# Kernel tuning notes

Hardware: AMD Instinct MI355X
Metric: run time of the kernel (lower is better)

The kernel has to match this reference:

```python
import jax, jax.numpy as jnp
import numpy as np

N = 768  # length of time vector

def setup_inputs() -> dict:
    key = jax.random.key(0)
    ks = jax.random.split(key, 4)
    # time vector (sorted grid-like values, as in a GP time axis)
    x = jnp.sort(jax.random.uniform(ks[0], (N,), dtype=jnp.float32) * (6 * np.pi))
    # MLP params: Linear(2,1024) -> Sigmoid -> Linear(1024,128) -> ReLU -> Linear(128,1)
    W1 = jax.random.normal(ks[1], (1024, 2), dtype=jnp.float32) * (1.0 / np.sqrt(2.0))
    b1 = jnp.zeros((1024,), dtype=jnp.float32)
    W2 = jax.random.normal(ks[2], (128, 1024), dtype=jnp.float32) * (1.0 / np.sqrt(1024.0))
    b2 = jnp.zeros((128,), dtype=jnp.float32)
    W3 = jax.random.normal(ks[3], (1, 128), dtype=jnp.float32) * (1.0 / np.sqrt(128.0))
    b3 = jnp.zeros((1,), dtype=jnp.float32)
    return {"x": x, "W1": W1, "b1": b1, "W2": W2, "b2": b2, "W3": W3, "b3": b3}


def reference(x, W1, b1, W2, b2, W3, b3):
    n = x.shape[0]
    # all (i, j) with j >= i  -> n(n+1)/2 pairs; replaces the Python double loop
    iu, ju = jnp.triu_indices(n)
    pairs = jnp.stack([x[iu], x[ju]], axis=-1)            # [P, 2]
    h = jax.nn.sigmoid(pairs @ W1.T + b1)                 # [P, 1024]
    h = jax.nn.relu(h @ W2.T + b2)                        # [P, 128]
    v = (h @ W3.T + b3)[:, 0]                             # [P]
    # K starts as eye; upper triangle INCLUDING diagonal is overwritten
    K = jnp.eye(n, dtype=x.dtype).at[iu, ju].set(v)       # [n, n] upper-triangular
    return K.T @ K                                        # symmetric PSD covariance
```

## Files before the change

kernel.cpp:

```cpp
#include <hip/hip_runtime.h>
#include <hip/hip_bf16.h>

#define NN 768
#define MD 1024
#define NPAIR 295296
#define NPBLK 1154

typedef __attribute__((ext_vector_type(8))) short s16x8;
typedef __attribute__((ext_vector_type(4))) float f32x4;
typedef __attribute__((ext_vector_type(2))) __bf16 b16x2;

__device__ __forceinline__ ushort bf16_rn(float f) {
    uint u = __builtin_bit_cast(uint, f);
    u += 0x7FFFu + ((u >> 16) & 1u);
    return (ushort)(u >> 16);
}

__device__ __forceinline__ void ptoij(int p, int& io, int& jo) {
    const float disc = (float)(1537 * 1537 - 8 * p);
    int i = (int)((1537.0f - sqrtf(disc)) * 0.5f);
    i = i < 0 ? 0 : (i > 767 ? 767 : i);
    while (i > 0 && p < i * (1537 - i) / 2) --i;
    while (i < 767 && p >= (i + 1) * (1536 - i) / 2) ++i;
    io = i;
    jo = i + (p - i * (1537 - i) / 2);
}

#define GLOAD16(gsrc, ldst)                                                        \
    __builtin_amdgcn_global_load_lds(                                              \
        (const __attribute__((address_space(1))) void*)(gsrc),                     \
        (__attribute__((address_space(3))) void*)(ldst), 16, 0, 0)

__global__ __launch_bounds__(256) void w2bf16(const float* __restrict__ W2,
                                              ushort* __restrict__ WhiS)
{
    const int id = blockIdx.x * 256 + threadIdx.x;
    const int k = id >> 7;
    const int m = (id & 127) * 8;
    const float4 a = *reinterpret_cast<const float4*>(W2 + k * MD + m);
    const float4 b = *reinterpret_cast<const float4*>(W2 + k * MD + m + 4);
    const float w[8] = {a.x, a.y, a.z, a.w, b.x, b.y, b.z, b.w};
    s16x8 h;
#pragma unroll
    for (int e = 0; e < 8; ++e) h[e] = (short)bf16_rn(w[e]);
    const int c = m >> 6;
    const int mloc8 = (m >> 3) & 7;
    const int byte = (mloc8 * 16) ^ ((k & 7) << 4);
    const int off = c * 8192 + ((k * 128 + byte) >> 1);
    *reinterpret_cast<s16x8*>(&WhiS[off]) = h;
}

#define STAGE(cc, buf)                                                       \
    {                                                                        \
        const ushort* sh_ = WhiS + (cc) * 8192;                              \
        _Pragma("unroll")                                                    \
        for (int q_ = 0; q_ < 4; ++q_) {                                     \
            const int off_ = (wv * 4 + q_) * 512;                            \
            GLOAD16(sh_ + off_ + lane * 8, &Wh[buf][off_]);                  \
        }                                                                    \
    }

#define SIG_CHUNK(cc, dst)                                                   \
    {                                                                        \
        _Pragma("unroll")                                                    \
        for (int ks_ = 0; ks_ < 2; ++ks_) {                                  \
            const int m0_ = (cc) * 64 + ks_ * 32 + l4 * 8;                   \
            const f32x4 a0_ = *reinterpret_cast<const f32x4*>(&sa[m0_]);     \
            const f32x4 a1_ = *reinterpret_cast<const f32x4*>(&sa[m0_ + 4]); \
            const f32x4 c0_ = *reinterpret_cast<const f32x4*>(&sc[m0_]);     \
            const f32x4 c1_ = *reinterpret_cast<const f32x4*>(&sc[m0_ + 4]); \
            const f32x4 b0_ = *reinterpret_cast<const f32x4*>(&sb[m0_]);     \
            const f32x4 b1_ = *reinterpret_cast<const f32x4*>(&sb[m0_ + 4]); \
            _Pragma("unroll")                                                \
            for (int tm_ = 0; tm_ < 4; ++tm_) {                              \
                float s_[8];                                                 \
                _Pragma("unroll")                                            \
                for (int e_ = 0; e_ < 4; ++e_) {                             \
                    const float u0_ = fmaf(xia[tm_], a0_[e_], fmaf(xja[tm_], c0_[e_], b0_[e_])); \
                    const float u1_ = fmaf(xia[tm_], a1_[e_], fmaf(xja[tm_], c1_[e_], b1_[e_])); \
                    s_[e_]     = __builtin_amdgcn_rcpf(1.0f + __builtin_amdgcn_exp2f(u0_)); \
                    s_[e_ + 4] = __builtin_amdgcn_rcpf(1.0f + __builtin_amdgcn_exp2f(u1_)); \
                }                                                            \
                union { s16x8 v; uint u[4]; } fr_;                           \
                _Pragma("unroll")                                            \
                for (int h_ = 0; h_ < 4; ++h_) {                             \
                    b16x2 p_;                                                \
                    p_.x = (__bf16)s_[2 * h_];                               \
                    p_.y = (__bf16)s_[2 * h_ + 1];                           \
                    fr_.u[h_] = __builtin_bit_cast(uint, p_);                \
                }                                                            \
                dst[ks_][tm_] = fr_.v;                                       \
            }                                                                \
        }                                                                    \
    }

#define MFMA_STEP(buf, src)                                                  \
    {                                                                        \
        _Pragma("unroll")                                                    \
        for (int ks_ = 0; ks_ < 2; ++ks_) {                                  \
            _Pragma("unroll")                                                \
            for (int th_ = 0; th_ < 2; ++th_) {                              \
                s16x8 bh_[4];                                                \
                _Pragma("unroll")                                            \
                for (int tn_ = 0; tn_ < 4; ++tn_) {                          \
                    const int k_ = th_ * 64 + tn_ * 16 + l15;                \
                    const int byte_ = (ks_ * 64 + l4 * 16) ^ ((k_ & 7) << 4);\
                    const int idx_ = (k_ * 128 + byte_) >> 1;                \
                    bh_[tn_] = *reinterpret_cast<const s16x8*>(&Wh[buf][idx_]); \
                }                                                            \
                __builtin_amdgcn_s_setprio(1);                               \
                _Pragma("unroll")                                            \
                for (int tm_ = 0; tm_ < 4; ++tm_)                            \
                    _Pragma("unroll")                                        \
                    for (int tn_ = 0; tn_ < 4; ++tn_)                        \
                        acc[tm_][th_][tn_] = __builtin_amdgcn_mfma_f32_16x16x32_bf16( \
                            src[ks_][tm_], bh_[tn_], acc[tm_][th_][tn_], 0, 0, 0);    \
                __builtin_amdgcn_s_setprio(0);                               \
            }                                                                \
        }                                                                    \
    }

__global__ __launch_bounds__(256, 2) void mlp_pairs(
    const float* __restrict__ x,
    const float* __restrict__ W1, const float* __restrict__ b1,
    const ushort* __restrict__ WhiS,
    const float* __restrict__ b2, const float* __restrict__ W3,
    const float* __restrict__ b3, float* __restrict__ K)
{
    __shared__ __align__(16) float sa[MD], sc[MD], sb[MD];
    __shared__ __align__(16) ushort Wh[2][8192];

    const int t = threadIdx.x;
    const int lane = t & 63, wv = t >> 6;
    const int l15 = lane & 15, l4 = lane >> 4;

    const float NL2E = -1.4426950408889634f;
    for (int m = t; m < MD; m += 256) {
        const float2 w = reinterpret_cast<const float2*>(W1)[m];
        sa[m] = w.x * NL2E;
        sc[m] = w.y * NL2E;
        sb[m] = b1[m] * NL2E;
    }

    const int pairbase = blockIdx.x * 256 + wv * 64;

    float xia[4], xja[4];
#pragma unroll
    for (int tm = 0; tm < 4; ++tm) {
        const int p = pairbase + tm * 16 + l15;
        if (p < NPAIR) {
            int i, j;
            ptoij(p, i, j);
            xia[tm] = x[i];
            xja[tm] = x[j];
        } else {
            xia[tm] = 0.f;
            xja[tm] = 0.f;
        }
    }

    f32x4 acc[4][2][4];
#pragma unroll
    for (int a = 0; a < 4; ++a)
#pragma unroll
        for (int th = 0; th < 2; ++th)
#pragma unroll
            for (int b = 0; b < 4; ++b) acc[a][th][b] = (f32x4){0.f, 0.f, 0.f, 0.f};

    STAGE(0, 0);
    __syncthreads();

    s16x8 ah[2][4];
    for (int c = 0; c < 16; ++c) {
        if (c < 15) STAGE(c + 1, (c + 1) & 1);
        SIG_CHUNK(c, ah);
        MFMA_STEP(c & 1, ah);
        __syncthreads();
    }

    float w3v[2][4], b2v[2][4];
#pragma unroll
    for (int th = 0; th < 2; ++th)
#pragma unroll
        for (int tn = 0; tn < 4; ++tn) {
            const int k = th * 64 + tn * 16 + l15;
            w3v[th][tn] = W3[k];
            b2v[th][tn] = b2[k];
        }
    const float b3v = b3[0];
#pragma unroll
    for (int tm = 0; tm < 4; ++tm)
#pragma unroll
        for (int r = 0; r < 4; ++r) {
            float v = 0.f;
#pragma unroll
            for (int th = 0; th < 2; ++th)
#pragma unroll
                for (int tn = 0; tn < 4; ++tn)
                    v = fmaf(w3v[th][tn], fmaxf(acc[tm][th][tn][r] + b2v[th][tn], 0.f), v);
            v += __shfl_xor(v, 1, 16);
            v += __shfl_xor(v, 2, 16);
            v += __shfl_xor(v, 4, 16);
            v += __shfl_xor(v, 8, 16);
            if (l15 == 0) {
                const int p = pairbase + tm * 16 + l4 * 4 + r;
                if (p < NPAIR) {
                    int i, j;
                    ptoij(p, i, j);
                    K[i * NN + j] = v + b3v;
                }
            }
        }
}

#define MC 32
#define JT 128
#define SPAD 132
__global__ __launch_bounds__(256) void mlp_fill(
    const float* __restrict__ x,
    const float* __restrict__ W1, const float* __restrict__ b1,
    const float* __restrict__ W2, const float* __restrict__ b2,
    const float* __restrict__ W3, const float* __restrict__ b3,
    float* __restrict__ K)
{
    const int i  = blockIdx.y;
    const int j0 = blockIdx.x * JT;
    if (j0 + JT - 1 < i) return;
    __shared__ float sA[MD];
    __shared__ float sCw[MD];
    __shared__ float sxj[JT];
    __shared__ float S[MC][SPAD];
    __shared__ float W2t[MC][SPAD];
    const int t = threadIdx.x;
    const float xi = x[i];
    for (int m = t; m < MD; m += 256) {
        const float2 w = reinterpret_cast<const float2*>(W1)[m];
        sA[m]  = fmaf(xi, w.x, b1[m]);
        sCw[m] = w.y;
    }
    if (t < JT) sxj[t] = x[j0 + t];
    const int tk = t & 15;
    const int tj = t >> 4;
    float w3r[8], b2r[8];
#pragma unroll
    for (int kk = 0; kk < 8; kk++) {
        w3r[kk] = W3[tk * 8 + kk];
        b2r[kk] = b2[tk * 8 + kk];
    }
    float acc[8][8];
#pragma unroll
    for (int jj = 0; jj < 8; jj++)
#pragma unroll
        for (int kk = 0; kk < 8; kk++) acc[jj][kk] = 0.f;
    const int jx   = t & 127;
    const int mseg = (t >> 7) * 16;
    __syncthreads();
    const float xjv = sxj[jx];
    for (int m0 = 0; m0 < MD; m0 += MC) {
#pragma unroll
        for (int q = 0; q < 4; q++) {
            const int f   = t + q * 256;
            const int k   = f >> 3;
            const int mm4 = (f & 7) * 4;
            const float4 w = *reinterpret_cast<const float4*>(W2 + k * MD + m0 + mm4);
            W2t[mm4 + 0][k] = w.x;
            W2t[mm4 + 1][k] = w.y;
            W2t[mm4 + 2][k] = w.z;
            W2t[mm4 + 3][k] = w.w;
        }
#pragma unroll
        for (int q = 0; q < 16; q++) {
            const int ml = mseg + q;
            const float z = fmaf(xjv, sCw[m0 + ml], sA[m0 + ml]);
            S[ml][jx] = 1.0f / (1.0f + __expf(-z));
        }
        __syncthreads();
#pragma unroll 4
        for (int mm = 0; mm < MC; mm++) {
            const float4 s0 = *reinterpret_cast<const float4*>(&S[mm][tj * 8]);
            const float4 s1 = *reinterpret_cast<const float4*>(&S[mm][tj * 8 + 4]);
            const float4 w0 = *reinterpret_cast<const float4*>(&W2t[mm][tk * 8]);
            const float4 w1 = *reinterpret_cast<const float4*>(&W2t[mm][tk * 8 + 4]);
            const float sj[8] = {s0.x, s0.y, s0.z, s0.w, s1.x, s1.y, s1.z, s1.w};
            const float wk[8] = {w0.x, w0.y, w0.z, w0.w, w1.x, w1.y, w1.z, w1.w};
#pragma unroll
            for (int jj = 0; jj < 8; jj++)
#pragma unroll
                for (int kk = 0; kk < 8; kk++)
                    acc[jj][kk] = fmaf(sj[jj], wk[kk], acc[jj][kk]);
        }
        __syncthreads();
    }
    const float b3v = b3[0];
#pragma unroll
    for (int jj = 0; jj < 8; jj++) {
        float v = 0.f;
#pragma unroll
        for (int kk = 0; kk < 8; kk++) {
            const float h = acc[jj][kk] + b2r[kk];
            v = fmaf(w3r[kk], fmaxf(h, 0.f), v);
        }
#pragma unroll
        for (int off = 8; off >= 1; off >>= 1)
            v += __shfl_xor(v, off, 16);
        if (tk == 0) {
            const int j = j0 + tj * 8 + jj;
            if (j >= i) K[i * NN + j] = v + b3v;
        }
    }
}

__global__ __launch_bounds__(256) void ktk(const float* __restrict__ K,
                                           float* __restrict__ C)
{
    const int b0 = blockIdx.x * 64;
    const int a0 = blockIdx.y * 64;
    __shared__ float Ka[64][68];
    __shared__ float Kb[64][68];
    const int t  = threadIdx.x;
    const int tb = t & 15;
    const int ta = t >> 4;
    float acc[4][4];
#pragma unroll
    for (int u = 0; u < 4; u++)
#pragma unroll
        for (int v = 0; v < 4; v++) acc[u][v] = 0.f;
    const int kmax = (a0 < b0 ? a0 : b0) + 64;
    for (int k0 = 0; k0 < kmax; k0 += 64) {
#pragma unroll
        for (int q = 0; q < 4; q++) {
            const int f  = t + q * 256;
            const int kk = f >> 4;
            const int c4 = (f & 15) * 4;
            *reinterpret_cast<float4*>(&Ka[kk][c4]) =
                *reinterpret_cast<const float4*>(K + (k0 + kk) * NN + a0 + c4);
            *reinterpret_cast<float4*>(&Kb[kk][c4]) =
                *reinterpret_cast<const float4*>(K + (k0 + kk) * NN + b0 + c4);
        }
        __syncthreads();
#pragma unroll 8
        for (int kk = 0; kk < 64; kk++) {
            const float4 av = *reinterpret_cast<const float4*>(&Ka[kk][ta * 4]);
            const float4 bv = *reinterpret_cast<const float4*>(&Kb[kk][tb * 4]);
            const float a4[4] = {av.x, av.y, av.z, av.w};
            const float b4[4] = {bv.x, bv.y, bv.z, bv.w};
#pragma unroll
            for (int u = 0; u < 4; u++)
#pragma unroll
                for (int v = 0; v < 4; v++)
                    acc[u][v] = fmaf(a4[u], b4[v], acc[u][v]);
        }
        __syncthreads();
    }
#pragma unroll
    for (int u = 0; u < 4; u++) {
        float4 o;
        o.x = acc[u][0]; o.y = acc[u][1]; o.z = acc[u][2]; o.w = acc[u][3];
        *reinterpret_cast<float4*>(C + (a0 + ta * 4 + u) * NN + b0 + tb * 4) = o;
    }
}

extern "C" void kernel_launch(void* const* d_in, const int* in_sizes, int n_in,
                              void* d_out, int out_size, void* d_ws, size_t ws_size,
                              hipStream_t stream)
{
    const float* x  = (const float*)d_in[0];
    const float* W1 = (const float*)d_in[1];
    const float* b1 = (const float*)d_in[2];
    const float* W2 = (const float*)d_in[3];
    const float* b2 = (const float*)d_in[4];
    const float* W3 = (const float*)d_in[5];
    const float* b3 = (const float*)d_in[6];
    float* Kmat = (float*)d_ws;
    float* C    = (float*)d_out;

    const size_t kBytes = (size_t)NN * NN * sizeof(float);
    const size_t need   = kBytes + 262144;

    hipMemsetAsync(Kmat, 0, kBytes, stream);
    if (ws_size >= need) {
        ushort* WhiS = (ushort*)((char*)d_ws + kBytes);
        w2bf16<<<64, 256, 0, stream>>>(W2, WhiS);
        mlp_pairs<<<NPBLK, 256, 0, stream>>>(x, W1, b1, WhiS, b2, W3, b3, Kmat);
    } else {
        mlp_fill<<<dim3(6, NN), 256, 0, stream>>>(x, W1, b1, W2, b2, W3, b3, Kmat);
    }
    ktk<<<dim3(NN / 64, NN / 64), 256, 0, stream>>>(Kmat, C);
}
```

Baseline: 188.7 us.

## Factor sigmoid exponentials into per-point tables to drop per-pair exp

Since exp(-(a*xi + c*xj + b)) factors as exp(-(a*xi+b)) * exp(-c*xj), a new pre-kernel builds two 768x1024 tables of these factors. The pair kernel then forms each sigmoid as rcp(fma(EA,EC,1)), which removes the per-element exp2 and the FMAs that built the argument. The cost is that each pair now gathers its operands from global memory tables (about 6 MB in total, mostly cached) instead of reading weights from LDS. It also adds an extra launch, raises the workspace requirement, and drops the scalar fallback path, so nothing fills K if the workspace is too small.

Measured after the change: 342.6 us. +81.5%, slower.

```diff
diff --git a/kernel.cpp b/kernel.cpp
--- a/kernel.cpp
+++ b/kernel.cpp
@@ -50,6 +50,22 @@
     *reinterpret_cast<s16x8*>(&WhiS[off]) = h;
 }
 
+__global__ __launch_bounds__(256) void etab(const float* __restrict__ x,
+                                            const float* __restrict__ W1,
+                                            const float* __restrict__ b1,
+                                            float* __restrict__ EA,
+                                            float* __restrict__ EC)
+{
+    const int i = blockIdx.x;
+    const float xi = x[i];
+    const float NL2E = -1.4426950408889634f;
+    for (int m = threadIdx.x; m < MD; m += 256) {
+        const float2 w = reinterpret_cast<const float2*>(W1)[m];
+        EA[i * MD + m] = __builtin_amdgcn_exp2f(fmaf(w.x, xi, b1[m]) * NL2E);
+        EC[i * MD + m] = __builtin_amdgcn_exp2f(w.y * xi * NL2E);
+    }
+}
+
 #define STAGE(cc, buf)                                                       \
     {                                                                        \
         const ushort* sh_ = WhiS + (cc) * 8192;                              \
@@ -57,6 +73,64 @@
         for (int q_ = 0; q_ < 4; ++q_) {                                     \
             const int off_ = (wv * 4 + q_) * 512;                            \
             GLOAD16(sh_ + off_ + lane * 8, &Wh[buf][off_]);                  \
+        }                                                                    \
+    }
+
+#define SIG_CHUNK2(cc, dst)                                                  \
+    {                                                                        \
+        _Pragma("unroll")                                                    \
+        for (int ks_ = 0; ks_ < 2; ++ks_) {                                  \
+            const int mo_ = (cc) * 64 + ks_ * 32;                            \
+            _Pragma("unroll")                                                \
+            for (int tm_ = 0; tm_ < 4; ++tm_) {                              \
+                const float* pa_ = pEA[tm_] + mo_;                           \
+                const float* pc_ = pEC[tm_] + mo_;                           \
+                const f32x4 ea0_ = *reinterpret_cast<const f32x4*>(pa_);     \
+                const f32x4 ea1_ = *reinterpret_cast<const f32x4*>(pa_ + 4); \
+                const f32x4 ec0_ = *reinterpret_cast<const f32x4*>(pc_);     \
+                const f32x4 ec1_ = *reinterpret_cast<const f32x4*>(pc_ + 4); \
+                float s_[8];                                                 \
+                _Pragma("unroll")                                            \
+                for (int e_ = 0; e_ < 4; ++e_) {                             \
+                    s_[e_]     = __builtin_amdgcn_rcpf(fmaf(ea0_[e_], ec0_[e_], 1.0f)); \
+                    s_[e_ + 4] = __builtin_amdgcn_rcpf(fmaf(ea1_[e_], ec1_[e_], 1.0f)); \
+                }                                                            \
+                union { s16x8 v; uint u[4]; } fr_;                           \
+                _Pragma("unroll")                                            \
+                for (int h_ = 0; h_ < 4; ++h_) {                             \
+                    b16x2 p_;                                                \
+                    p_.x = (__bf16)s_[2 * h_];                               \
+                    p_.y = (__bf16)s_[2 * h_ + 1];                           \
+                    fr_.u[h_] = __builtin_bit_cast(uint, p_);                \
+                }                                                            \
+                dst[ks_][tm_] = fr_.v;                                       \
+            }                                                                \
+        }                                                                    \
+    }
+
+#define MFMA_STEP(buf, src)                                                  \
+    {                                                                        \
+        _Pragma("unroll")                                                    \
+        for (int ks_ = 0; ks_ < 2; ++ks_) {                                  \
+            _Pragma("unroll")                                                \
+            for (int th_ = 0; th_ < 2; ++th_) {                              \
+                s16x8 bh_[4];                                                \
+                _Pragma("unroll")                                            \
+                for (int tn_ = 0; tn_ < 4; ++tn_) {                          \
+                    const int k_ = th_ * 64 + tn_ * 16 + l15;                \
+                    const int byte_ = (ks_ * 64 + l4 * 16) ^ ((k_ & 7) << 4);\
+                    const int idx_ = (k_ * 128 + byte_) >> 1;                \
+                    bh_[tn_] = *reinterpret_cast<const s16x8*>(&Wh[buf][idx_]); \
+                }                                                            \
+                __builtin_amdgcn_s_setprio(1);                               \
+                _Pragma("unroll")                                            \
+                for (int tm_ = 0; tm_ < 4; ++tm_)                            \
+                    _Pragma("unroll")                                        \
+                    for (int tn_ = 0; tn_ < 4; ++tn_)                        \
+                        acc[tm_][th_][tn_] = __builtin_amdgcn_mfma_f32_16x16x32_bf16( \
+                            src[ks_][tm_], bh_[tn_], acc[tm_][th_][tn_], 0, 0, 0);    \
+                __builtin_amdgcn_s_setprio(0);                               \
+            }                                                                \
         }                                                                    \
     }
 
@@ -94,69 +168,30 @@
         }                                                                    \
     }
 
-#define MFMA_STEP(buf, src)                                                  \
-    {                                                                        \
-        _Pragma("unroll")                                                    \
-        for (int ks_ = 0; ks_ < 2; ++ks_) {                                  \
-            _Pragma("unroll")                                                \
-            for (int th_ = 0; th_ < 2; ++th_) {                              \
-                s16x8 bh_[4];                                                \
-                _Pragma("unroll")                                            \
-                for (int tn_ = 0; tn_ < 4; ++tn_) {                          \
-                    const int k_ = th_ * 64 + tn_ * 16 + l15;                \
-                    const int byte_ = (ks_ * 64 + l4 * 16) ^ ((k_ & 7) << 4);\
-                    const int idx_ = (k_ * 128 + byte_) >> 1;                \
-                    bh_[tn_] = *reinterpret_cast<const s16x8*>(&Wh[buf][idx_]); \
-                }                                                            \
-                __builtin_amdgcn_s_setprio(1);                               \
-                _Pragma("unroll")                                            \
-                for (int tm_ = 0; tm_ < 4; ++tm_)                            \
-                    _Pragma("unroll")                                        \
-                    for (int tn_ = 0; tn_ < 4; ++tn_)                        \
-                        acc[tm_][th_][tn_] = __builtin_amdgcn_mfma_f32_16x16x32_bf16( \
-                            src[ks_][tm_], bh_[tn_], acc[tm_][th_][tn_], 0, 0, 0);    \
-                __builtin_amdgcn_s_setprio(0);                               \
-            }                                                                \
-        }                                                                    \
-    }
-
-__global__ __launch_bounds__(256, 2) void mlp_pairs(
-    const float* __restrict__ x,
-    const float* __restrict__ W1, const float* __restrict__ b1,
+__global__ __launch_bounds__(256, 2) void mlp_pairs2(
+    const float* __restrict__ EA, const float* __restrict__ EC,
     const ushort* __restrict__ WhiS,
     const float* __restrict__ b2, const float* __restrict__ W3,
     const float* __restrict__ b3, float* __restrict__ K)
 {
-    __shared__ __align__(16) float sa[MD], sc[MD], sb[MD];
     __shared__ __align__(16) ushort Wh[2][8192];
 
     const int t = threadIdx.x;
     const int lane = t & 63, wv = t >> 6;
     const int l15 = lane & 15, l4 = lane >> 4;
 
-    const float NL2E = -1.4426950408889634f;
-    for (int m = t; m < MD; m += 256) {
-        const float2 w = reinterpret_cast<const float2*>(W1)[m];
-        sa[m] = w.x * NL2E;
-        sc[m] = w.y * NL2E;
-        sb[m] = b1[m] * NL2E;
-    }
-
     const int pairbase = blockIdx.x * 256 + wv * 64;
 
-    float xia[4], xja[4];
+    const float* pEA[4];
+    const float* pEC[4];
 #pragma unroll
     for (int tm = 0; tm < 4; ++tm) {
-        const int p = pairbase + tm * 16 + l15;
-        if (p < NPAIR) {
-            int i, j;
-            ptoij(p, i, j);
-            xia[tm] = x[i];
-            xja[tm] = x[j];
-        } else {
-            xia[tm] = 0.f;
-            xja[tm] = 0.f;
-        }
+        int p = pairbase + tm * 16 + l15;
+        if (p >= NPAIR) p = 0;
+        int i, j;
+        ptoij(p, i, j);
+        pEA[tm] = EA + i * MD + l4 * 8;
+        pEC[tm] = EC + j * MD + l4 * 8;
     }
 
     f32x4 acc[4][2][4];
@@ -173,7 +208,7 @@
     s16x8 ah[2][4];
     for (int c = 0; c < 16; ++c) {
         if (c < 15) STAGE(c + 1, (c + 1) & 1);
-        SIG_CHUNK(c, ah);
+        SIG_CHUNK2(c, ah);
         MFMA_STEP(c & 1, ah);
         __syncthreads();
     }
@@ -213,101 +248,97 @@
         }
 }
 
-#define MC 32
-#define JT 128
-#define SPAD 132
-__global__ __launch_bounds__(256) void mlp_fill(
+__global__ __launch_bounds__(256, 2) void mlp_pairs(
     const float* __restrict__ x,
     const float* __restrict__ W1, const float* __restrict__ b1,
-    const float* __restrict__ W2, const float* __restrict__ b2,
-    const float* __restrict__ W3, const float* __restrict__ b3,
-    float* __restrict__ K)
-{
-    const int i  = blockIdx.y;
-    const int j0 = blockIdx.x * JT;
-    if (j0 + JT - 1 < i) return;
-    __shared__ float sA[MD];
-    __shared__ float sCw[MD];
-    __shared__ float sxj[JT];
-    __shared__ float S[MC][SPAD];
-    __shared__ float W2t[MC][SPAD];
+    const ushort* __restrict__ WhiS,
+    const float* __restrict__ b2, const float* __restrict__ W3,
+    const float* __restrict__ b3, float* __restrict__ K)
+{
+    __shared__ __align__(16) float sa[MD], sc[MD], sb[MD];
+    __shared__ __align__(16) ushort Wh[2][8192];
+
     const int t = threadIdx.x;
-    const float xi = x[i];
+    const int lane = t & 63, wv = t >> 6;
+    const int l15 = lane & 15, l4 = lane >> 4;
+
+    const float NL2E = -1.4426950408889634f;
     for (int m = t; m < MD; m += 256) {
         const float2 w = reinterpret_cast<const float2*>(W1)[m];
-        sA[m]  = fmaf(xi, w.x, b1[m]);
-        sCw[m] = w.y;
-    }
-    if (t < JT) sxj[t] = x[j0 + t];
-    const int tk = t & 15;
-    const int tj = t >> 4;
-    float w3r[8], b2r[8];
-#pragma unroll
-    for (int kk = 0; kk < 8; kk++) {
-        w3r[kk] = W3[tk * 8 + kk];
-        b2r[kk] = b2[tk * 8 + kk];
-    }
-    float acc[8][8];
-#pragma unroll
-    for (int jj = 0; jj < 8; jj++)
-#pragma unroll
-        for (int kk = 0; kk < 8; kk++) acc[jj][kk] = 0.f;
-    const int jx   = t & 127;
-    const int mseg = (t >> 7) * 16;
+        sa[m] = w.x * NL2E;
+        sc[m] = w.y * NL2E;
+        sb[m] = b1[m] * NL2E;
+    }
+
+    const int pairbase = blockIdx.x * 256 + wv * 64;
+
+    float xia[4], xja[4];
+#pragma unroll
+    for (int tm = 0; tm < 4; ++tm) {
+        const int p = pairbase + tm * 16 + l15;
+        if (p < NPAIR) {
+            int i, j;
+            ptoij(p, i, j);
+            xia[tm] = x[i];
+            xja[tm] = x[j];
+        } else {
+            xia[tm] = 0.f;
+            xja[tm] = 0.f;
+        }
+    }
+
+    f32x4 acc[4][2][4];
+#pragma unroll
+    for (int a = 0; a < 4; ++a)
+#pragma unroll
+        for (int th = 0; th < 2; ++th)
+#pragma unroll
+            for (int b = 0; b < 4; ++b) acc[a][th][b] = (f32x4){0.f, 0.f, 0.f, 0.f};
+
+    STAGE(0, 0);
     __syncthreads();
-    const float xjv = sxj[jx];
-    for (int m0 = 0; m0 < MD; m0 += MC) {
-#pragma unroll
-        for (int q = 0; q < 4; q++) {
-            const int f   = t + q * 256;
-            const int k   = f >> 3;
-            const int mm4 = (f & 7) * 4;
-            const float4 w = *reinterpret_cast<const float4*>(W2 + k * MD + m0 + mm4);
-            W2t[mm4 + 0][k] = w.x;
-            W2t[mm4 + 1][k] = w.y;
-            W2t[mm4 + 2][k] = w.z;
-            W2t[mm4 + 3][k] = w.w;
-        }
-#pragma unroll
-        for (int q = 0; q < 16; q++) {
-            const int ml = mseg + q;
-            const float z = fmaf(xjv, sCw[m0 + ml], sA[m0 + ml]);
-            S[ml][jx] = 1.0f / (1.0f + __expf(-z));
-        }
+
+    s16x8 ah[2][4];
+    for (int c = 0; c < 16; ++c) {
+        if (c < 15) STAGE(c + 1, (c + 1) & 1);
+        SIG_CHUNK(c, ah);
+        MFMA_STEP(c & 1, ah);
         __syncthreads();
-#pragma unroll 4
-        for (int mm = 0; mm < MC; mm++) {
-            const float4 s0 = *reinterpret_cast<const float4*>(&S[mm][tj * 8]);
-            const float4 s1 = *reinterpret_cast<const float4*>(&S[mm][tj * 8 + 4]);
-            const float4 w0 = *reinterpret_cast<const float4*>(&W2t[mm][tk * 8]);
-            const float4 w1 = *reinterpret_cast<const float4*>(&W2t[mm][tk * 8 + 4]);
-            const float sj[8] = {s0.x, s0.y, s0.z, s0.w, s1.x, s1.y, s1.z, s1.w};
-            const float wk[8] = {w0.x, w0.y, w0.z, w0.w, w1.x, w1.y, w1.z, w1.w};
-#pragma unroll
-            for (int jj = 0; jj < 8; jj++)
-#pragma unroll
-                for (int kk = 0; kk < 8; kk++)
-                    acc[jj][kk] = fmaf(sj[jj], wk[kk], acc[jj][kk]);
-        }
-        __syncthreads();
-    }
+    }
+
+    float w3v[2][4], b2v[2][4];
+#pragma unroll
+    for (int th = 0; th < 2; ++th)
+#pragma unroll
+        for (int tn = 0; tn < 4; ++tn) {
+            const int k = th * 64 + tn * 16 + l15;
+            w3v[th][tn] = W3[k];
+            b2v[th][tn] = b2[k];
+        }
     const float b3v = b3[0];
 #pragma unroll
-    for (int jj = 0; jj < 8; jj++) {
-        float v = 0.f;
-#pragma unroll
-        for (int kk = 0; kk < 8; kk++) {
-            const float h = acc[jj][kk] + b2r[kk];
-            v = fmaf(w3r[kk], fmaxf(h, 0.f), v);
-        }
-#pragma unroll
-        for (int off = 8; off >= 1; off >>= 1)
-            v += __shfl_xor(v, off, 16);
-        if (tk == 0) {
-            const int j = j0 + tj * 8 + jj;
-            if (j >= i) K[i * NN + j] = v + b3v;
-        }
-    }
+    for (int tm = 0; tm < 4; ++tm)
+#pragma unroll
+        for (int r = 0; r < 4; ++r) {
+            float v = 0.f;
+#pragma unroll
+            for (int th = 0; th < 2; ++th)
+#pragma unroll
+                for (int tn = 0; tn < 4; ++tn)
+                    v = fmaf(w3v[th][tn], fmaxf(acc[tm][th][tn][r] + b2v[th][tn], 0.f), v);
+            v += __shfl_xor(v, 1, 16);
+            v += __shfl_xor(v, 2, 16);
+            v += __shfl_xor(v, 4, 16);
+            v += __shfl_xor(v, 8, 16);
+            if (l15 == 0) {
+                const int p = pairbase + tm * 16 + l4 * 4 + r;
+                if (p < NPAIR) {
+                    int i, j;
+                    ptoij(p, i, j);
+                    K[i * NN + j] = v + b3v;
+                }
+            }
+        }
 }
 
 __global__ __launch_bounds__(256) void ktk(const float* __restrict__ K,
@@ -374,16 +405,24 @@
     float* Kmat = (float*)d_ws;
     float* C    = (float*)d_out;
 
-    const size_t kBytes = (size_t)NN * NN * sizeof(float);
-    const size_t need   = kBytes + 262144;
+    const size_t kBytes  = (size_t)NN * NN * sizeof(float);
+    const size_t wBytes  = 262144;
+    const size_t tBytes  = (size_t)NN * MD * sizeof(float);
+    const size_t needTab = kBytes + wBytes + 2 * tBytes;
+    const size_t needR5  = kBytes + wBytes;
 
     hipMemsetAsync(Kmat, 0, kBytes, stream);
-    if (ws_size >= need) {
+    if (ws_size >= needTab) {
+        ushort* WhiS = (ushort*)((char*)d_ws + kBytes);
+        float*  EA   = (float*)((char*)d_ws + kBytes + wBytes);
+        float*  EC   = EA + NN * MD;
+        w2bf16<<<64, 256, 0, stream>>>(W2, WhiS);
+        etab<<<NN, 256, 0, stream>>>(x, W1, b1, EA, EC);
+        mlp_pairs2<<<NPBLK, 256, 0, stream>>>(EA, EC, WhiS, b2, W3, b3, Kmat);
+    } else if (ws_size >= needR5) {
         ushort* WhiS = (ushort*)((char*)d_ws + kBytes);
         w2bf16<<<64, 256, 0, stream>>>(W2, WhiS);
         mlp_pairs<<<NPBLK, 256, 0, stream>>>(x, W1, b1, WhiS, b2, W3, b3, Kmat);
-    } else {
-        mlp_fill<<<dim3(6, NN), 256, 0, stream>>>(x, W1, b1, W2, b2, W3, b3, Kmat);
     }
     ktk<<<dim3(NN / 64, NN / 64), 256, 0, stream>>>(Kmat, C);
 }
```
